# Kernel tuning notes

Measured on AMD Instinct MI355X. Metric: run time of the kernel, lower is better.

The kernel has to match this reference:

```python
import jax, jax.numpy as jnp
import numpy as np
import math

D_MODEL = 1024
EXPAND = 2
D_INNER = D_MODEL * EXPAND  # 2048
D_STATE = 16
DT_RANK = max(1, (D_MODEL + 15) // 16)  # 64
K = 4  # conv kernel size
B, S = 2, 2048


def silu(v):
    return v * jax.nn.sigmoid(v)


def setup_inputs() -> dict:
    key = jax.random.key(0)
    ks = jax.random.split(key, 12)
    sc = lambda fan_in: 1.0 / math.sqrt(fan_in)
    x = jax.random.normal(ks[0], (B, S, D_MODEL), dtype=jnp.float32)
    Win = jax.random.normal(ks[1], (D_MODEL, 2 * D_INNER), dtype=jnp.float32) * sc(D_MODEL)
    Wconv = jax.random.normal(ks[2], (D_INNER, 1, K), dtype=jnp.float32) * sc(K)
    bconv = jax.random.normal(ks[3], (D_INNER,), dtype=jnp.float32) * 0.01
    Wx = jax.random.normal(ks[4], (D_INNER, DT_RANK + 2 * D_STATE), dtype=jnp.float32) * sc(D_INNER)
    Wdt = jax.random.normal(ks[5], (DT_RANK, D_INNER), dtype=jnp.float32) * sc(DT_RANK)
    # dt_proj bias init: inverse-softplus of dt ~ LogUniform[1e-3, 1e-1]
    dt = jnp.exp(jax.random.uniform(ks[6], (D_INNER,)) * (math.log(0.1) - math.log(0.001)) + math.log(0.001))
    dt = jnp.clip(dt, 0.0001, None)
    bdt = dt + jnp.log(-jnp.expm1(-dt))
    a = jnp.arange(1, D_STATE + 1, dtype=jnp.float32)[None, :].repeat(D_INNER, axis=0)
    a = a + jax.random.uniform(ks[7], a.shape) * 0.1
    A_log = jnp.log(a)
    Dp = jnp.ones((D_INNER,), dtype=jnp.float32)
    Wout = jax.random.normal(ks[8], (D_INNER, D_MODEL), dtype=jnp.float32) * sc(D_INNER)
    return {"x": x, "Win": Win, "Wconv": Wconv, "bconv": bconv, "Wx": Wx,
            "Wdt": Wdt, "bdt": bdt, "A_log": A_log, "Dp": Dp, "Wout": Wout}


def causal_dw_conv(x, Wconv, bconv):
    # x: [B, S, C] -> depthwise causal conv along S
    xc = jnp.transpose(x, (0, 2, 1))  # [B, C, S]
    y = jax.lax.conv_general_dilated(
        xc, Wconv, window_strides=(1,), padding=[(K - 1, 0)],
        feature_group_count=D_INNER,
        dimension_numbers=("NCH", "OIH", "NCH"))
    y = y + bconv[None, :, None]
    return jnp.transpose(y, (0, 2, 1))  # [B, S, C]


def selective_scan(u, delta, b_term, c_term, A_log, Dp):
    # u, delta: [B,S,Di]; b_term, c_term: [B,S,Ds]
    a = -jnp.exp(A_log)  # [Di, Ds]
    delta_a = jnp.exp(delta[..., None] * a[None, None])            # [B,S,Di,Ds] fp32
    delta_b_u = (delta * u)[..., None] * b_term[:, :, None, :]     # [B,S,Di,Ds]
    du = u * Dp[None, None, :]                                     # [B,S,Di]
    # time-major for scan
    dA = jnp.transpose(delta_a, (1, 0, 2, 3))
    dBu = jnp.transpose(delta_b_u, (1, 0, 2, 3))
    c_t = jnp.transpose(c_term, (1, 0, 2))
    du_t = jnp.transpose(du, (1, 0, 2))

    def step(state, inp):
        dA_t, dBu_t, c, duv = inp
        state = dA_t * state + dBu_t                  # [B,Di,Ds]
        y = jnp.einsum("bdn,bn->bd", state, c) + duv  # [B,Di]
        return state, y

    init = jnp.zeros((u.shape[0], D_INNER, D_STATE), dtype=jnp.float32)
    _, ys = jax.lax.scan(step, init, (dA, dBu, c_t, du_t))
    return jnp.transpose(ys, (1, 0, 2))  # [B,S,Di]


def reference(x, Win, Wconv, bconv, Wx, Wdt, bdt, A_log, Dp, Wout):
    xz = x @ Win                              # [B,S,2*Di]
    x_branch, z_branch = jnp.split(xz, 2, axis=-1)
    x_branch = silu(causal_dw_conv(x_branch, Wconv, bconv))
    params = x_branch @ Wx                    # [B,S,R+2*Ds]
    delta, b_term, c_term = jnp.split(params, [DT_RANK, DT_RANK + D_STATE], axis=-1)
    delta = jax.nn.softplus(delta @ Wdt + bdt)
    y = selective_scan(x_branch, delta, b_term, c_term, A_log, Dp)
    y = y * silu(z_branch)
    return y @ Wout
```

## Files before the change

### kernel.cpp

```cpp
#include <hip/hip_runtime.h>

typedef unsigned short u16;
typedef _Float16 f16;
typedef f16 f16x8 __attribute__((ext_vector_type(8)));
typedef u16 u16x8 __attribute__((ext_vector_type(8)));
typedef short s16x8 __attribute__((ext_vector_type(8)));
typedef float f32x2 __attribute__((ext_vector_type(2)));
typedef float f32x4 __attribute__((ext_vector_type(4)));
typedef float f32x8 __attribute__((ext_vector_type(8)));

#define T_TOK 4096
#define B_SZ 2
#define S_LEN 2048
#define DMODEL 1024
#define DI 2048
#define DS 16
#define RNK 64
#define NCH 64
#define CLEN 32
#define LDXZ 4096
#define SK 8
#define SK4 4
#define PRM_SLICE (4096 * 128)
#define OUT_SLICE (4096 * 1024)
#define LOG2E 1.4426950408889634f

#define GLOAD_LDS16(gp, lp)                                                                   \
  __builtin_amdgcn_global_load_lds((const __attribute__((address_space(1))) void*)(gp),       \
                                   (__attribute__((address_space(3))) void*)(lp), 16, 0, 0)

__device__ __forceinline__ float b2f(u16 v) { return __uint_as_float(((unsigned)v) << 16); }
__device__ __forceinline__ u16 f2b(float f) {
  unsigned u = __float_as_uint(f);
  return (u16)((u + 0x7fffu + ((u >> 16) & 1u)) >> 16);
}
__device__ __forceinline__ float fexp2(float x) {
#if __has_builtin(__builtin_amdgcn_exp2f)
  return __builtin_amdgcn_exp2f(x);
#else
  return exp2f(x);
#endif
}
__device__ __forceinline__ int dtype_of(const void* dp) {
  unsigned v = *(const unsigned*)dp;
  return (v == 0x3F800000u) ? 0 : (v == 0x3C003C00u) ? 2 : 1;
}
__device__ __forceinline__ float load_any(const void* p, size_t i, int flag) {
  if (flag == 0) return ((const float*)p)[i];
  if (flag == 1) return b2f(((const u16*)p)[i]);
  return (float)((const f16*)p)[i];
}

__device__ __forceinline__ void tr_tile(const void* __restrict__ src, void* __restrict__ dst,
                                        int R, int C, int Cpad, int f, int bx, int by, int ob) {
  __shared__ f16 t[32][33];
  int c0 = bx * 32, r0 = by * 32;
  int tx = threadIdx.x & 31, ty = threadIdx.x >> 5;
#pragma unroll
  for (int i = ty; i < 32; i += 8) {
    int r = r0 + i, c = c0 + tx;
    float v = (r < R && c < C) ? load_any(src, (size_t)r * C + c, f) : 0.f;
    t[i][tx] = (f16)v;
  }
  __syncthreads();
#pragma unroll
  for (int i = ty; i < 32; i += 8) {
    int c = c0 + i, r = r0 + tx;
    if (c < Cpad && r < R) {
      if (ob) ((u16*)dst)[(size_t)c * R + r] = f2b((float)t[tx][i]);
      else ((f16*)dst)[(size_t)c * R + r] = t[tx][i];
    }
  }
}

__global__ __launch_bounds__(256) void k_prep(const void* __restrict__ Wconv, const void* __restrict__ bconv,
                                              const void* __restrict__ bdt, const void* __restrict__ A_log,
                                              const void* __restrict__ Dp, const void* __restrict__ Wx,
                                              const void* __restrict__ Wdt, const void* __restrict__ Win,
                                              const void* __restrict__ x, f16* __restrict__ WxT,
                                              f16* __restrict__ WdtT, u16* __restrict__ WinTb,
                                              u16* __restrict__ xhb, float* __restrict__ a_f,
                                              float* __restrict__ wconv_f, float* __restrict__ bconv_f,
                                              float* __restrict__ bdt_f, float* __restrict__ dp_f,
                                              int* __restrict__ flag) {
  int f = dtype_of(Dp);
  int bid = blockIdx.x, t = threadIdx.x;
  if (bid < 128) {
    int i = bid * 256 + t;
    a_f[i] = -__expf(load_any(A_log, i, f)) * LOG2E;
  } else if (bid < 160) {
    int i = (bid - 128) * 256 + t;
    wconv_f[i] = load_any(Wconv, i, f);
  } else if (bid < 168) {
    int i = (bid - 160) * 256 + t;
    bconv_f[i] = load_any(bconv, i, f);
  } else if (bid < 176) {
    int i = (bid - 168) * 256 + t;
    bdt_f[i] = load_any(bdt, i, f);
  } else if (bid < 184) {
    int i = (bid - 176) * 256 + t;
    dp_f[i] = load_any(Dp, i, f);
  } else if (bid == 184) {
    if (t == 0) *flag = f;
  } else if (bid < 441) {
    int id = bid - 185;
    tr_tile(Wx, WxT, 2048, 96, 128, f, id & 3, id >> 2, 0);
  } else if (bid < 569) {
    int id = bid - 441;
    tr_tile(Wdt, WdtT, 64, 2048, 2048, f, id & 63, id >> 6, 0);
  } else if (bid < 4665) {
    int id = bid - 569;
    tr_tile(Win, WinTb, 1024, 4096, 4096, f, id & 127, id >> 7, 1);
  } else {
    if (f == 1) return;
    size_t i = (size_t)(bid - 4665) * 2048 + (size_t)t * 8;
    u16x8 o;
    if (f == 0) {
      const float* s = (const float*)x + i;
#pragma unroll
      for (int j = 0; j < 8; ++j) o[j] = f2b(s[j]);
    } else {
      const f16* s = (const f16*)x + i;
#pragma unroll
      for (int j = 0; j < 8; ++j) o[j] = f2b((float)s[j]);
    }
    *(u16x8*)(xhb + i) = o;
  }
}

__global__ __launch_bounds__(256) void k_transpose16(const void* __restrict__ src, f16* __restrict__ dst,
                                                     int R, int C, int Cpad, const void* __restrict__ Dp) {
  tr_tile(src, dst, R, C, Cpad, dtype_of(Dp), blockIdx.x, blockIdx.y, 0);
}

__global__ __launch_bounds__(512) void k_gemm1(const void* __restrict__ x0, const u16* __restrict__ xhb,
                                               const u16* __restrict__ Bw, f16* __restrict__ C,
                                               const int* __restrict__ flag) {
  constexpr int LD = 1024, LDC = LDXZ, NT = 16, NP = NT / 2;
  __shared__ __align__(16) u16 lds[8 * 8192];
  const u16* A = (*flag == 1) ? (const u16*)x0 : xhb;
  const int tid = threadIdx.x;
  const int wv = tid >> 6, ln = tid & 63;
  const int quad = ln >> 4, l16 = ln & 15;
  const int wr = wv >> 2, wc = wv & 3;
  const int m0 = blockIdx.y * 256, n0 = blockIdx.x * 256;
  const int rr = tid >> 3;
  const int cc = (tid & 7) ^ (rr & 7);
  const u16* aBase = A + (size_t)m0 * LD + cc * 8;
  const u16* bBase = Bw + (size_t)n0 * LD + cc * 8;
  const int brow = ((tid >> 8) << 6) + (rr & 31);
  u16* const dBase = lds + wv * 512;
  auto stageA = [&](int tile, int mq) {
    const u16* s = aBase + (size_t)(mq * 64 + rr) * LD + tile * 64;
    u16* d = dBase + ((tile & 1) * 4 + mq) * 8192;
    GLOAD_LDS16(s, d);
    GLOAD_LDS16(s + 128 * LD, d + 4096);
  };
  auto stageB = [&](int tile, int nq) {
    const u16* s = bBase + (size_t)(brow + nq * 32) * LD + tile * 64;
    u16* d = dBase + ((tile & 1) * 4 + 2 + nq) * 8192;
    GLOAD_LDS16(s, d);
    GLOAD_LDS16(s + 128 * LD, d + 4096);
  };
  const int rxor = (l16 & 7) << 3;
  f32x4 acc[8][4] = {};
  stageA(0, 0); stageB(0, 1); stageB(0, 0); stageA(0, 1);
  stageA(1, 0); stageB(1, 1);
  asm volatile("s_waitcnt vmcnt(4)" ::: "memory");
  __builtin_amdgcn_s_barrier();
  s16x8 af[4][2], bf[2][2];
  for (int pr = 0; pr < NP; ++pr) {
    const int t0 = 2 * pr;
    const bool more = (pr < NP - 1);
#pragma unroll
    for (int ph = 0; ph < 8; ++ph) {
      const int slot = ph >> 2, q = ph & 3;
      const int mq = q >> 1, nq = (q >> 1) ^ (q & 1);
      const u16* Ar = lds + (slot * 4 + mq) * 8192;
      const u16* Br = lds + (slot * 4 + 2 + nq) * 8192;
      if (q == 0 || q == 2) {
#pragma unroll
        for (int i = 0; i < 4; ++i) {
          const int ra = wr * 64 + i * 16 + l16;
#pragma unroll
          for (int kk = 0; kk < 2; ++kk)
            af[i][kk] = *(const s16x8*)(Ar + ra * 64 + ((kk * 32 + quad * 8) ^ rxor));
        }
      }
      if (q != 2) {
#pragma unroll
        for (int j = 0; j < 2; ++j) {
          const int rb = wc * 32 + j * 16 + l16;
#pragma unroll
          for (int kk = 0; kk < 2; ++kk)
            bf[j][kk] = *(const s16x8*)(Br + rb * 64 + ((kk * 32 + quad * 8) ^ rxor));
        }
      }
      if (ph == 0) stageB(t0 + 1, 0);
      else if (ph == 1) stageA(t0 + 1, 1);
      else if (more) {
        if (ph == 2) stageA(t0 + 2, 0);
        else if (ph == 3) stageB(t0 + 2, 1);
        else if (ph == 4) stageB(t0 + 2, 0);
        else if (ph == 5) stageA(t0 + 2, 1);
        else if (ph == 6) stageA(t0 + 3, 0);
        else stageB(t0 + 3, 1);
      }
      __builtin_amdgcn_s_barrier();
      asm volatile("s_waitcnt lgkmcnt(0)" ::: "memory");
      __builtin_amdgcn_sched_barrier(0);
      __builtin_amdgcn_s_setprio(1);
#pragma unroll
      for (int kk = 0; kk < 2; ++kk)
#pragma unroll
        for (int i = 0; i < 4; ++i)
#pragma unroll
          for (int j = 0; j < 2; ++j)
            acc[mq * 4 + i][nq * 2 + j] = __builtin_amdgcn_mfma_f32_16x16x32_bf16(
                af[i][kk], bf[j][kk], acc[mq * 4 + i][nq * 2 + j], 0, 0, 0);
      __builtin_amdgcn_s_setprio(0);
      if (ph == 3) {
        if (more) asm volatile("s_waitcnt vmcnt(6)" ::: "memory");
        else asm volatile("s_waitcnt vmcnt(2)" ::: "memory");
      } else if (ph == 5) {
        if (more) asm volatile("s_waitcnt vmcnt(8)" ::: "memory");
        else asm volatile("s_waitcnt vmcnt(0)" ::: "memory");
      } else if (ph == 7) {
        if (more) asm volatile("s_waitcnt vmcnt(4)" ::: "memory");
        else asm volatile("s_waitcnt vmcnt(0)" ::: "memory");
      }
      __builtin_amdgcn_s_barrier();
    }
  }
#pragma unroll
  for (int i = 0; i < 8; ++i)
#pragma unroll
    for (int j = 0; j < 4; ++j)
#pragma unroll
      for (int r = 0; r < 4; ++r) {
        const int row = m0 + wr * 128 + i * 16 + quad * 4 + r;
        const int col = n0 + wc * 64 + j * 16 + l16;
        C[(size_t)row * LDC + col] = (f16)acc[i][j][r];
      }
}

template <int BM, int BN, int EPI>
__global__ __launch_bounds__(256) void k_gemm2(const f16* __restrict__ A, const f16* __restrict__ B,
                                               void* __restrict__ Cv, const float* __restrict__ bias,
                                               const int* __restrict__ flag,
                                               int klen, int lda, int ldb, int ldc) {
  constexpr int WM = BM / 2, WN = BN / 2;
  constexpr int FM = WM / 16, FN = WN / 16;
  __shared__ __align__(16) f16 As[2 * BM * 32];
  __shared__ __align__(16) f16 Bs[2 * BN * 32];
  const int tid = threadIdx.x;
  const int wv = tid >> 6, ln = tid & 63;
  const int quad = ln >> 4, l16 = ln & 15;
  const int lrow = ln >> 2;
  const int lch = (((ln & 3) ^ ((ln >> 3) & 3))) * 8;
  const int m0 = blockIdx.y * BM, n0 = blockIdx.x * BN;
  const int wm = (wv & 1) * WM, wn = (wv >> 1) * WN;
  const int kbase = blockIdx.z * klen;
  const int qsw = (quad ^ ((l16 >> 1) & 3)) * 8;
  f32x4 acc[FM][FN] = {};
  for (int kk = 0; kk < klen; kk += 64) {
    const int k0 = kbase + kk;
    __syncthreads();
#pragma unroll
    for (int h = 0; h < 2; ++h) {
#pragma unroll
      for (int i = 0; i < BM / 64; ++i) {
        int r0 = wv * (BM / 4) + i * 16;
        GLOAD_LDS16(A + (size_t)(m0 + r0 + lrow) * lda + k0 + h * 32 + lch, As + h * BM * 32 + r0 * 32);
      }
#pragma unroll
      for (int i = 0; i < BN / 64; ++i) {
        int r0 = wv * (BN / 4) + i * 16;
        GLOAD_LDS16(B + (size_t)(n0 + r0 + lrow) * ldb + k0 + h * 32 + lch, Bs + h * BN * 32 + r0 * 32);
      }
    }
    __syncthreads();
#pragma unroll
    for (int h = 0; h < 2; ++h) {
      f16x8 af[FM], bf[FN];
#pragma unroll
      for (int i = 0; i < FM; ++i) af[i] = *(const f16x8*)(As + h * BM * 32 + (wm + i * 16 + l16) * 32 + qsw);
#pragma unroll
      for (int j = 0; j < FN; ++j) bf[j] = *(const f16x8*)(Bs + h * BN * 32 + (wn + j * 16 + l16) * 32 + qsw);
#pragma unroll
      for (int i = 0; i < FM; ++i)
#pragma unroll
        for (int j = 0; j < FN; ++j)
          acc[i][j] = __builtin_amdgcn_mfma_f32_16x16x32_f16(af[i], bf[j], acc[i][j], 0, 0, 0);
    }
  }
  int dflag = 1;
  if constexpr (EPI == 2) dflag = *flag;
  f16* Cz = (f16*)Cv;
  if constexpr (EPI == 4) Cz = (f16*)Cv + (size_t)blockIdx.z * PRM_SLICE;
  if constexpr (EPI == 5) Cz = (f16*)Cv + (size_t)blockIdx.z * OUT_SLICE;
#pragma unroll
  for (int i = 0; i < FM; ++i)
#pragma unroll
    for (int j = 0; j < FN; ++j)
#pragma unroll
      for (int r = 0; r < 4; ++r) {
        int row = m0 + wm + i * 16 + quad * 4 + r;
        int col = n0 + wn + j * 16 + l16;
        size_t ci = (size_t)row * ldc + col;
        float v = acc[i][j][r];
        if constexpr (EPI == 3) {
          v += bias[row];
          v = (v > 20.f) ? v : log1pf(__expf(v));
          size_t di2 = ((size_t)(row << 1) + (col >> 11)) * (size_t)LDXZ + (col & 2047);
          Cz[di2] = (f16)v;
        } else if constexpr (EPI == 2) {
          if (dflag == 0) ((float*)Cv)[ci] = v;
          else if (dflag == 1) ((u16*)Cv)[ci] = f2b(v);
          else ((f16*)Cv)[ci] = (f16)v;
        } else {
          Cz[ci] = (f16)v;
        }
      }
}

__global__ __launch_bounds__(256) void k_sum_prm(const f16* __restrict__ parts, f16* __restrict__ prm,
                                                 float* __restrict__ prmBC) {
  size_t i = (size_t)(blockIdx.x * 256 + threadIdx.x) * 8;
  int col0 = (int)(i & 127);
  if (col0 >= 96) return;
  float s[8] = {};
#pragma unroll
  for (int z = 0; z < SK; ++z) {
    f16x8 v = *(const f16x8*)(parts + (size_t)z * PRM_SLICE + i);
#pragma unroll
    for (int j = 0; j < 8; ++j) s[j] += (float)v[j];
  }
  if (col0 < 64) {
    f16x8 o;
#pragma unroll
    for (int j = 0; j < 8; ++j) o[j] = (f16)s[j];
    *(f16x8*)(prm + i) = o;
  } else {
    size_t tok = i >> 7;
    f32x8 of;
#pragma unroll
    for (int j = 0; j < 8; ++j) of[j] = s[j];
    *(f32x8*)(prmBC + tok * 32 + (col0 - 64)) = of;
  }
}

__global__ __launch_bounds__(256) void k_sum_out(const f16* __restrict__ parts, void* __restrict__ out,
                                                 const int* __restrict__ flag) {
  size_t i = (size_t)(blockIdx.x * 256 + threadIdx.x) * 8;
  float s[8] = {};
#pragma unroll
  for (int z = 0; z < SK4; ++z) {
    f16x8 v = *(const f16x8*)(parts + (size_t)z * OUT_SLICE + i);
#pragma unroll
    for (int j = 0; j < 8; ++j) s[j] += (float)v[j];
  }
  int f = *flag;
  if (f == 0) {
    f32x8 o;
#pragma unroll
    for (int j = 0; j < 8; ++j) o[j] = s[j];
    *(f32x8*)((float*)out + i) = o;
  } else if (f == 1) {
    u16x8 o;
#pragma unroll
    for (int j = 0; j < 8; ++j) o[j] = f2b(s[j]);
    *(u16x8*)((u16*)out + i) = o;
  } else {
    f16x8 o;
#pragma unroll
    for (int j = 0; j < 8; ++j) o[j] = (f16)s[j];
    *(f16x8*)((f16*)out + i) = o;
  }
}

__global__ __launch_bounds__(256) void k_conv_silu(const f16* __restrict__ xz, const float* __restrict__ Wconv,
                                                   const float* __restrict__ bconv, f16* __restrict__ xc) {
  int t = blockIdx.x;
  int s = t & (S_LEN - 1);
  int d8 = threadIdx.x * 8;
  float w[4][8];
#pragma unroll
  for (int i = 0; i < 8; ++i)
#pragma unroll
    for (int j = 0; j < 4; ++j) w[j][i] = Wconv[(d8 + i) * 4 + j];
  float acc[8];
#pragma unroll
  for (int i = 0; i < 8; ++i) acc[i] = bconv[d8 + i];
#pragma unroll
  for (int j = 0; j < 4; ++j) {
    int sl = s - 3 + j;
    if (sl >= 0) {
      f16x8 xv = *(const f16x8*)(xz + (size_t)(t - 3 + j) * LDXZ + d8);
#pragma unroll
      for (int i = 0; i < 8; ++i) acc[i] = fmaf((float)xv[i], w[j][i], acc[i]);
    }
  }
  f16x8 o;
#pragma unroll
  for (int i = 0; i < 8; ++i) {
    float v = acc[i];
    o[i] = (f16)(v / (1.f + __expf(-v)));
  }
  *(f16x8*)(xc + (size_t)t * DI + d8) = o;
}

__global__ __launch_bounds__(256) void k_scan_passA(const f16* __restrict__ dltT, const f16* __restrict__ u,
                                                    const float* __restrict__ prmBC, const float* __restrict__ a_f,
                                                    f16* __restrict__ lcs, float* __restrict__ sumdv) {
  __shared__ __align__(16) f16 u_lds[CLEN][128];
  __shared__ __align__(16) float b_lds[CLEN][16];
  const int tid = threadIdx.x;
  int g = blockIdx.x * 256 + tid;
  int nh = g & 1, p = g >> 1;
  int d = p & (DI - 1);
  int c = (p >> 11) & (NCH - 1);
  int b = p >> 17;
  const int d0 = d & ~127;
  const int t0 = b * S_LEN + c * CLEN;
  {
    const f16* up0 = u + (size_t)t0 * DI + d0;
#pragma unroll
    for (int rep = 0; rep < 2; ++rep) {
      int chunk = rep * 256 + tid;
      int row = chunk >> 4, c16 = chunk & 15;
      *(f16x8*)&u_lds[row][c16 * 8] = *(const f16x8*)(up0 + (size_t)row * DI + c16 * 8);
    }
    const float* bp0 = prmBC + (size_t)t0 * 32;
    int row = tid >> 3, c2 = tid & 7;
    *(f32x2*)&b_lds[row][c2 * 2] = *(const f32x2*)(bp0 + row * 32 + c2 * 2);
  }
  const f16* dp = dltT + (size_t)(2 * d + b) * LDXZ + c * CLEN;
  f16x8 dlv[4];
#pragma unroll
  for (int q = 0; q < 4; ++q) dlv[q] = *(const f16x8*)(dp + q * 8);
  f32x4 a0 = *(const f32x4*)(a_f + d * DS + nh * 8);
  f32x4 a1 = *(const f32x4*)(a_f + d * DS + nh * 8 + 4);
  float a[8] = {a0[0], a0[1], a0[2], a0[3], a1[0], a1[1], a1[2], a1[3]};
  __syncthreads();
  const int dd = d - d0;
  float st[8] = {};
  float sumd = 0.f;
#pragma unroll
  for (int s = 0; s < CLEN; ++s) {
    float dl = (float)dlv[s >> 3][s & 7];
    float uv = (float)u_lds[s][dd];
    f32x4 bv0 = *(const f32x4*)&b_lds[s][nh * 8];
    f32x4 bv1 = *(const f32x4*)&b_lds[s][nh * 8 + 4];
    sumd += dl;
    float dbu = dl * uv;
#pragma unroll
    for (int j = 0; j < 8; ++j) {
      float e = fexp2(dl * a[j]);
      float bj = (j < 4) ? bv0[j & 3] : bv1[j & 3];
      st[j] = fmaf(e, st[j], dbu * bj);
    }
  }
  f16x8 o;
#pragma unroll
  for (int j = 0; j < 8; ++j) o[j] = (f16)st[j];
  *(f16x8*)(lcs + (size_t)p * DS + nh * 8) = o;
  if (nh == 0) sumdv[p] = sumd;
}

__global__ __launch_bounds__(256) void k_scan_passB(f16* __restrict__ lcs, const float* __restrict__ sumdv,
                                                    const float* __restrict__ a_f) {
  int g = blockIdx.x * 256 + threadIdx.x;
  int n = g & 15, d = (g >> 4) & (DI - 1), b = g >> 15;
  float an = a_f[d * DS + n];
  const size_t base = (size_t)b * NCH * DI + d;
  float lf[4], sf[4];
#pragma unroll
  for (int q = 0; q < 4; ++q) {
    size_t pq = base + (size_t)q * DI;
    lf[q] = (float)lcs[pq * DS + n];
    sf[q] = sumdv[pq];
  }
  float init = 0.f;
#pragma unroll
  for (int c = 0; c < NCH; ++c) {
    size_t pc = base + (size_t)c * DI;
    float l = lf[c & 3], sd = sf[c & 3];
    if (c + 4 < NCH) {
      size_t pn = base + (size_t)(c + 4) * DI;
      lf[c & 3] = (float)lcs[pn * DS + n];
      sf[c & 3] = sumdv[pn];
    }
    lcs[pc * DS + n] = (f16)init;
    init = fexp2(sd * an) * init + l;
  }
}

__global__ __launch_bounds__(256) void k_scan_passC(const f16* __restrict__ dltT, const f16* __restrict__ u,
                                                    const float* __restrict__ prmBC, const float* __restrict__ a_f,
                                                    const float* __restrict__ dp_f, const f16* __restrict__ lcs,
                                                    f16* __restrict__ xz) {
  __shared__ __align__(16) f16 u_lds[CLEN][128];
  __shared__ __align__(16) f16 z_lds[CLEN][128];
  __shared__ __align__(16) float bc_lds[CLEN][32];
  const int tid = threadIdx.x;
  int g = blockIdx.x * 256 + tid;
  int nh = g & 1, p = g >> 1;
  int d = p & (DI - 1);
  int c = (p >> 11) & (NCH - 1);
  int b = p >> 17;
  const int d0 = d & ~127;
  const int t0 = b * S_LEN + c * CLEN;
  f16* const zp0 = xz + (size_t)t0 * LDXZ + DI + d0;
  {
    const f16* up0 = u + (size_t)t0 * DI + d0;
#pragma unroll
    for (int rep = 0; rep < 2; ++rep) {
      int chunk = rep * 256 + tid;
      int row = chunk >> 4, c16 = chunk & 15;
      *(f16x8*)&u_lds[row][c16 * 8] = *(const f16x8*)(up0 + (size_t)row * DI + c16 * 8);
      *(f16x8*)&z_lds[row][c16 * 8] = *(const f16x8*)(zp0 + (size_t)row * LDXZ + c16 * 8);
    }
    ((f32x4*)bc_lds)[tid] = ((const f32x4*)(prmBC + (size_t)t0 * 32))[tid];
  }
  const f16* dp = dltT + (size_t)(2 * d + b) * LDXZ + c * CLEN;
  f16x8 dlv[4];
#pragma unroll
  for (int q = 0; q < 4; ++q) dlv[q] = *(const f16x8*)(dp + q * 8);
  f32x4 a0 = *(const f32x4*)(a_f + d * DS + nh * 8);
  f32x4 a1 = *(const f32x4*)(a_f + d * DS + nh * 8 + 4);
  float a[8] = {a0[0], a0[1], a0[2], a0[3], a1[0], a1[1], a1[2], a1[3]};
  float st[8];
  f16x8 iv = *(const f16x8*)(lcs + (size_t)p * DS + nh * 8);
#pragma unroll
  for (int j = 0; j < 8; ++j) st[j] = (float)iv[j];
  float dpv = dp_f[d];
  __syncthreads();
  const int dd = d - d0;
#pragma unroll
  for (int s = 0; s < CLEN; ++s) {
    float dl = (float)dlv[s >> 3][s & 7];
    float uv = (float)u_lds[s][dd];
    float z = (float)z_lds[s][dd];
    f32x4 bv0 = *(const f32x4*)&bc_lds[s][nh * 8];
    f32x4 bv1 = *(const f32x4*)&bc_lds[s][nh * 8 + 4];
    f32x4 cv0 = *(const f32x4*)&bc_lds[s][16 + nh * 8];
    f32x4 cv1 = *(const f32x4*)&bc_lds[s][16 + nh * 8 + 4];
    float dbu = dl * uv;
    float part = (nh == 0) ? uv * dpv : 0.f;
#pragma unroll
    for (int j = 0; j < 8; ++j) {
      float e = fexp2(dl * a[j]);
      float bj = (j < 4) ? bv0[j & 3] : bv1[j & 3];
      float cj = (j < 4) ? cv0[j & 3] : cv1[j & 3];
      st[j] = fmaf(e, st[j], dbu * bj);
      part = fmaf(st[j], cj, part);
    }
    part += __shfl_xor(part, 1, 64);
    if (nh == 0) {
      float sg = 1.f / (1.f + __expf(-z));
      z_lds[s][dd] = (f16)(part * z * sg);
    }
  }
  __syncthreads();
#pragma unroll
  for (int rep = 0; rep < 2; ++rep) {
    int chunk = rep * 256 + tid;
    int row = chunk >> 4, c16 = chunk & 15;
    *(f16x8*)(zp0 + (size_t)row * LDXZ + c16 * 8) = *(const f16x8*)&z_lds[row][c16 * 8];
  }
}

extern "C" void kernel_launch(void* const* d_in, const int* in_sizes, int n_in,
                              void* d_out, int out_size, void* d_ws, size_t ws_size,
                              hipStream_t stream) {
  const void* x = d_in[0];
  const void* Win = d_in[1];
  const void* Wconv = d_in[2];
  const void* bconv = d_in[3];
  const void* Wx = d_in[4];
  const void* Wdt = d_in[5];
  const void* bdt = d_in[6];
  const void* A_log = d_in[7];
  const void* Dp = d_in[8];
  const void* Wout = d_in[9];
  (void)in_sizes; (void)n_in; (void)out_size; (void)ws_size;

  const size_t KB = 1024, MB = 1024 * 1024;
  char* ws = (char*)d_ws;
  f16* xzh = (f16*)ws;
  u16* xhb = (u16*)(ws + 32 * MB);
  f16* xch = (f16*)(ws + 32 * MB);
  u16* WinTb = (u16*)(ws + 48 * MB);
  f16* parts = (f16*)(ws + 48 * MB);
  f16* lcs = (f16*)(ws + 48 * MB);
  f16* WoutT = (f16*)(ws + 48 * MB);
  float* sumd = (float*)(ws + 56 * MB);
  f16* prm = (f16*)(ws + 57 * MB);
  float* prmBC = (float*)(ws + 58 * MB);
  f16* WxT = (f16*)(ws + 58 * MB + 512 * KB);
  f16* WdtT = (f16*)(ws + 59 * MB);
  float* a_f = (float*)(ws + 59 * MB + 256 * KB);
  float* wconv_f = (float*)(ws + 59 * MB + 384 * KB);
  float* bconv_f = (float*)(ws + 59 * MB + 416 * KB);
  float* bdt_f = (float*)(ws + 59 * MB + 424 * KB);
  float* dp_f = (float*)(ws + 59 * MB + 432 * KB);
  int* flag = (int*)(ws + 59 * MB + 440 * KB);
  f16* parts4 = (f16*)(ws + 64 * MB);

  k_prep<<<6713, 256, 0, stream>>>(Wconv, bconv, bdt, A_log, Dp, Wx, Wdt, Win, x,
                                   WxT, WdtT, WinTb, xhb, a_f, wconv_f, bconv_f, bdt_f, dp_f, flag);

  k_gemm1<<<dim3(16, 16), 512, 0, stream>>>(x, xhb, WinTb, xzh, flag);
  k_conv_silu<<<T_TOK, 256, 0, stream>>>(xzh, wconv_f, bconv_f, xch);
  k_gemm2<64, 128, 4><<<dim3(1, 4096 / 64, SK), 256, 0, stream>>>(
      xch, WxT, parts, nullptr, flag, 2048 / SK, 2048, 2048, 128);
  k_sum_prm<<<PRM_SLICE / 8 / 256, 256, 0, stream>>>(parts, prm, prmBC);
  k_gemm2<128, 128, 3><<<dim3(4096 / 128, 2048 / 128), 256, 0, stream>>>(
      WdtT, prm, xzh, bdt_f, flag, 64, 64, 128, 0);
  k_scan_passA<<<(B_SZ * NCH * DI * 2) / 256, 256, 0, stream>>>(xzh, xch, prmBC, a_f, lcs, sumd);
  k_scan_passB<<<(B_SZ * DI * DS) / 256, 256, 0, stream>>>(lcs, sumd, a_f);
  k_scan_passC<<<(B_SZ * NCH * DI * 2) / 256, 256, 0, stream>>>(xzh, xch, prmBC, a_f, dp_f, lcs, xzh);
  k_transpose16<<<dim3(1024 / 32, 2048 / 32), 256, 0, stream>>>(Wout, WoutT, 2048, 1024, 1024, Dp);
  k_gemm2<64, 128, 5><<<dim3(1024 / 128, 4096 / 64, SK4), 256, 0, stream>>>(
      xzh + DI, WoutT, parts4, nullptr, flag, 2048 / SK4, LDXZ, 2048, 1024);
  k_sum_out<<<OUT_SLICE / 8 / 256, 256, 0, stream>>>(parts4, d_out, flag);
}
```

Measured before the change: 330.8 us.

## Scan passes: one thread per channel with all 16 states, B/C via scalar loads

Scan passes A and C change from two threads per channel (8 states each, joined by a shuffle) to one thread per channel holding all 16 states, with each block covering 256 channels. B/C coefficients are read straight from global memory at block-uniform addresses, which can become scalar loads, instead of being staged in LDS. This removes the cross-lane shuffle, the nh-predicated work and the LDS traffic for B/C. In exchange the grid is half as large and each thread carries more registers, so there is less parallelism and possibly lower occupancy.

```diff
diff --git a/kernel.cpp b/kernel.cpp
--- a/kernel.cpp
+++ b/kernel.cpp
@@ -413,59 +413,57 @@
 __global__ __launch_bounds__(256) void k_scan_passA(const f16* __restrict__ dltT, const f16* __restrict__ u,
                                                     const float* __restrict__ prmBC, const float* __restrict__ a_f,
                                                     f16* __restrict__ lcs, float* __restrict__ sumdv) {
-  __shared__ __align__(16) f16 u_lds[CLEN][128];
-  __shared__ __align__(16) float b_lds[CLEN][16];
+  __shared__ __align__(16) f16 u_lds[CLEN][256];
   const int tid = threadIdx.x;
-  int g = blockIdx.x * 256 + tid;
-  int nh = g & 1, p = g >> 1;
-  int d = p & (DI - 1);
-  int c = (p >> 11) & (NCH - 1);
-  int b = p >> 17;
-  const int d0 = d & ~127;
+  const int blk = blockIdx.x;
+  const int dblk = blk & 7;
+  const int c = (blk >> 3) & (NCH - 1);
+  const int b = blk >> 9;
+  const int d = dblk * 256 + tid;
   const int t0 = b * S_LEN + c * CLEN;
   {
-    const f16* up0 = u + (size_t)t0 * DI + d0;
-#pragma unroll
-    for (int rep = 0; rep < 2; ++rep) {
+    const f16* up0 = u + (size_t)t0 * DI + dblk * 256;
+#pragma unroll
+    for (int rep = 0; rep < 4; ++rep) {
       int chunk = rep * 256 + tid;
-      int row = chunk >> 4, c16 = chunk & 15;
-      *(f16x8*)&u_lds[row][c16 * 8] = *(const f16x8*)(up0 + (size_t)row * DI + c16 * 8);
-    }
-    const float* bp0 = prmBC + (size_t)t0 * 32;
-    int row = tid >> 3, c2 = tid & 7;
-    *(f32x2*)&b_lds[row][c2 * 2] = *(const f32x2*)(bp0 + row * 32 + c2 * 2);
-  }
+      int row = chunk >> 5, c32 = chunk & 31;
+      *(f16x8*)&u_lds[row][c32 * 8] = *(const f16x8*)(up0 + (size_t)row * DI + c32 * 8);
+    }
+  }
+  const float* __restrict__ bcp = prmBC + (size_t)t0 * 32;
   const f16* dp = dltT + (size_t)(2 * d + b) * LDXZ + c * CLEN;
   f16x8 dlv[4];
 #pragma unroll
   for (int q = 0; q < 4; ++q) dlv[q] = *(const f16x8*)(dp + q * 8);
-  f32x4 a0 = *(const f32x4*)(a_f + d * DS + nh * 8);
-  f32x4 a1 = *(const f32x4*)(a_f + d * DS + nh * 8 + 4);
-  float a[8] = {a0[0], a0[1], a0[2], a0[3], a1[0], a1[1], a1[2], a1[3]};
+  float a[16];
+#pragma unroll
+  for (int q = 0; q < 4; ++q) {
+    f32x4 av = *(const f32x4*)(a_f + d * DS + q * 4);
+#pragma unroll
+    for (int j = 0; j < 4; ++j) a[q * 4 + j] = av[j];
+  }
   __syncthreads();
-  const int dd = d - d0;
-  float st[8] = {};
+  float st[16] = {};
   float sumd = 0.f;
 #pragma unroll
   for (int s = 0; s < CLEN; ++s) {
     float dl = (float)dlv[s >> 3][s & 7];
-    float uv = (float)u_lds[s][dd];
-    f32x4 bv0 = *(const f32x4*)&b_lds[s][nh * 8];
-    f32x4 bv1 = *(const f32x4*)&b_lds[s][nh * 8 + 4];
+    float uv = (float)u_lds[s][tid];
     sumd += dl;
     float dbu = dl * uv;
 #pragma unroll
-    for (int j = 0; j < 8; ++j) {
+    for (int j = 0; j < 16; ++j) {
       float e = fexp2(dl * a[j]);
-      float bj = (j < 4) ? bv0[j & 3] : bv1[j & 3];
-      st[j] = fmaf(e, st[j], dbu * bj);
-    }
-  }
-  f16x8 o;
-#pragma unroll
-  for (int j = 0; j < 8; ++j) o[j] = (f16)st[j];
-  *(f16x8*)(lcs + (size_t)p * DS + nh * 8) = o;
-  if (nh == 0) sumdv[p] = sumd;
+      st[j] = fmaf(e, st[j], dbu * bcp[s * 32 + j]);
+    }
+  }
+  size_t p = (size_t)b * NCH * DI + (size_t)c * DI + d;
+  f16x8 o0, o1;
+#pragma unroll
+  for (int j = 0; j < 8; ++j) { o0[j] = (f16)st[j]; o1[j] = (f16)st[j + 8]; }
+  *(f16x8*)(lcs + p * DS) = o0;
+  *(f16x8*)(lcs + p * DS + 8) = o1;
+  sumdv[p] = sumd;
 }
 
 __global__ __launch_bounds__(256) void k_scan_passB(f16* __restrict__ lcs, const float* __restrict__ sumdv,
@@ -500,74 +498,70 @@
                                                     const float* __restrict__ prmBC, const float* __restrict__ a_f,
                                                     const float* __restrict__ dp_f, const f16* __restrict__ lcs,
                                                     f16* __restrict__ xz) {
-  __shared__ __align__(16) f16 u_lds[CLEN][128];
-  __shared__ __align__(16) f16 z_lds[CLEN][128];
-  __shared__ __align__(16) float bc_lds[CLEN][32];
+  __shared__ __align__(16) f16 u_lds[CLEN][256];
+  __shared__ __align__(16) f16 z_lds[CLEN][256];
   const int tid = threadIdx.x;
-  int g = blockIdx.x * 256 + tid;
-  int nh = g & 1, p = g >> 1;
-  int d = p & (DI - 1);
-  int c = (p >> 11) & (NCH - 1);
-  int b = p >> 17;
-  const int d0 = d & ~127;
+  const int blk = blockIdx.x;
+  const int dblk = blk & 7;
+  const int c = (blk >> 3) & (NCH - 1);
+  const int b = blk >> 9;
+  const int d = dblk * 256 + tid;
   const int t0 = b * S_LEN + c * CLEN;
-  f16* const zp0 = xz + (size_t)t0 * LDXZ + DI + d0;
+  f16* const zp0 = xz + (size_t)t0 * LDXZ + DI + dblk * 256;
   {
-    const f16* up0 = u + (size_t)t0 * DI + d0;
-#pragma unroll
-    for (int rep = 0; rep < 2; ++rep) {
+    const f16* up0 = u + (size_t)t0 * DI + dblk * 256;
+#pragma unroll
+    for (int rep = 0; rep < 4; ++rep) {
       int chunk = rep * 256 + tid;
-      int row = chunk >> 4, c16 = chunk & 15;
-      *(f16x8*)&u_lds[row][c16 * 8] = *(const f16x8*)(up0 + (size_t)row * DI + c16 * 8);
-      *(f16x8*)&z_lds[row][c16 * 8] = *(const f16x8*)(zp0 + (size_t)row * LDXZ + c16 * 8);
-    }
-    ((f32x4*)bc_lds)[tid] = ((const f32x4*)(prmBC + (size_t)t0 * 32))[tid];
-  }
+      int row = chunk >> 5, c32 = chunk & 31;
+      *(f16x8*)&u_lds[row][c32 * 8] = *(const f16x8*)(up0 + (size_t)row * DI + c32 * 8);
+      *(f16x8*)&z_lds[row][c32 * 8] = *(const f16x8*)(zp0 + (size_t)row * LDXZ + c32 * 8);
+    }
+  }
+  const float* __restrict__ bcp = prmBC + (size_t)t0 * 32;
   const f16* dp = dltT + (size_t)(2 * d + b) * LDXZ + c * CLEN;
   f16x8 dlv[4];
 #pragma unroll
   for (int q = 0; q < 4; ++q) dlv[q] = *(const f16x8*)(dp + q * 8);
-  f32x4 a0 = *(const f32x4*)(a_f + d * DS + nh * 8);
-  f32x4 a1 = *(const f32x4*)(a_f + d * DS + nh * 8 + 4);
-  float a[8] = {a0[0], a0[1], a0[2], a0[3], a1[0], a1[1], a1[2], a1[3]};
-  float st[8];
-  f16x8 iv = *(const f16x8*)(lcs + (size_t)p * DS + nh * 8);
-#pragma unroll
-  for (int j = 0; j < 8; ++j) st[j] = (float)iv[j];
-  float dpv = dp_f[d];
+  float a[16];
+#pragma unroll
+  for (int q = 0; q < 4; ++q) {
+    f32x4 av = *(const f32x4*)(a_f + d * DS + q * 4);
+#pragma unroll
+    for (int j = 0; j < 4; ++j) a[q * 4 + j] = av[j];
+  }
+  size_t p = (size_t)b * NCH * DI + (size_t)c * DI + d;
+  float st[16];
+  {
+    f16x8 iv0 = *(const f16x8*)(lcs + p * DS);
+    f16x8 iv1 = *(const f16x8*)(lcs + p * DS + 8);
+#pragma unroll
+    for (int j = 0; j < 8; ++j) { st[j] = (float)iv0[j]; st[j + 8] = (float)iv1[j]; }
+  }
+  const float dpv = dp_f[d];
   __syncthreads();
-  const int dd = d - d0;
 #pragma unroll
   for (int s = 0; s < CLEN; ++s) {
     float dl = (float)dlv[s >> 3][s & 7];
-    float uv = (float)u_lds[s][dd];
-    float z = (float)z_lds[s][dd];
-    f32x4 bv0 = *(const f32x4*)&bc_lds[s][nh * 8];
-    f32x4 bv1 = *(const f32x4*)&bc_lds[s][nh * 8 + 4];
-    f32x4 cv0 = *(const f32x4*)&bc_lds[s][16 + nh * 8];
-    f32x4 cv1 = *(const f32x4*)&bc_lds[s][16 + nh * 8 + 4];
+    float uv = (float)u_lds[s][tid];
+    float z = (float)z_lds[s][tid];
     float dbu = dl * uv;
-    float part = (nh == 0) ? uv * dpv : 0.f;
-#pragma unroll
-    for (int j = 0; j < 8; ++j) {
+    float part = uv * dpv;
+#pragma unroll
+    for (int j = 0; j < 16; ++j) {
       float e = fexp2(dl * a[j]);
-      float bj = (j < 4) ? bv0[j & 3] : bv1[j & 3];
-      float cj = (j < 4) ? cv0[j & 3] : cv1[j & 3];
-      st[j] = fmaf(e, st[j], dbu * bj);
-      part = fmaf(st[j], cj, part);
-    }
-    part += __shfl_xor(part, 1, 64);
-    if (nh == 0) {
-      float sg = 1.f / (1.f + __expf(-z));
-      z_lds[s][dd] = (f16)(part * z * sg);
-    }
+      st[j] = fmaf(e, st[j], dbu * bcp[s * 32 + j]);
+      part = fmaf(st[j], bcp[s * 32 + 16 + j], part);
+    }
+    float sg = 1.f / (1.f + __expf(-z));
+    z_lds[s][tid] = (f16)(part * z * sg);
   }
   __syncthreads();
 #pragma unroll
-  for (int rep = 0; rep < 2; ++rep) {
+  for (int rep = 0; rep < 4; ++rep) {
     int chunk = rep * 256 + tid;
-    int row = chunk >> 4, c16 = chunk & 15;
-    *(f16x8*)(zp0 + (size_t)row * LDXZ + c16 * 8) = *(const f16x8*)&z_lds[row][c16 * 8];
+    int row = chunk >> 5, c32 = chunk & 31;
+    *(f16x8*)(zp0 + (size_t)row * LDXZ + c32 * 8) = *(const f16x8*)&z_lds[row][c32 * 8];
   }
 }
 
@@ -618,9 +612,9 @@
   k_sum_prm<<<PRM_SLICE / 8 / 256, 256, 0, stream>>>(parts, prm, prmBC);
   k_gemm2<128, 128, 3><<<dim3(4096 / 128, 2048 / 128), 256, 0, stream>>>(
       WdtT, prm, xzh, bdt_f, flag, 64, 64, 128, 0);
-  k_scan_passA<<<(B_SZ * NCH * DI * 2) / 256, 256, 0, stream>>>(xzh, xch, prmBC, a_f, lcs, sumd);
+  k_scan_passA<<<B_SZ * NCH * (DI / 256), 256, 0, stream>>>(xzh, xch, prmBC, a_f, lcs, sumd);
   k_scan_passB<<<(B_SZ * DI * DS) / 256, 256, 0, stream>>>(lcs, sumd, a_f);
-  k_scan_passC<<<(B_SZ * NCH * DI * 2) / 256, 256, 0, stream>>>(xzh, xch, prmBC, a_f, dp_f, lcs, xzh);
+  k_scan_passC<<<B_SZ * NCH * (DI / 256), 256, 0, stream>>>(xzh, xch, prmBC, a_f, dp_f, lcs, xzh);
   k_transpose16<<<dim3(1024 / 32, 2048 / 32), 256, 0, stream>>>(Wout, WoutT, 2048, 1024, 1024, Dp);
   k_gemm2<64, 128, 5><<<dim3(1024 / 128, 4096 / 64, SK4), 256, 0, stream>>>(
       xzh + DI, WoutT, parts4, nullptr, flag, 2048 / SK4, LDXZ, 2048, 1024);
```

Result: slower. 343.9 us (+4.0%).

## Use 256x256 pipelined split-K GEMM kernel for output projection

Applied to the files above, without the earlier changes.

Replaces the 64x128 split-K output projection GEMM with a new 256x256-tile, 512-thread kernel. It stages tiles into LDS through direct global-to-LDS loads with double buffering, uses an 8-phase interleaved load/compute schedule, and raises wave priority around the MFMA blocks. The larger tiles are meant to improve data reuse and overlap memory traffic with compute. The trade-off is fewer blocks (256 rather than 2048) and heavy LDS use, which may hurt occupancy.

```diff
diff --git a/kernel.cpp b/kernel.cpp
--- a/kernel.cpp
+++ b/kernel.cpp
@@ -244,6 +244,118 @@
       }
 }
 
+__global__ __launch_bounds__(512) void k_gemm8p(const f16* __restrict__ A, const f16* __restrict__ B,
+                                                f16* __restrict__ Cp, int lda, int ldb, int ldc,
+                                                int ksl, int nt) {
+  __shared__ __align__(16) u16 lds[8 * 8192];
+  const int np = nt >> 1;
+  const int tid = threadIdx.x;
+  const int wv = tid >> 6, ln = tid & 63;
+  const int quad = ln >> 4, l16 = ln & 15;
+  const int wr = wv >> 2, wc = wv & 3;
+  const int m0 = blockIdx.y * 256, n0 = blockIdx.x * 256;
+  const int kbase = blockIdx.z * ksl;
+  const int rr = tid >> 3;
+  const int cc = (tid & 7) ^ (rr & 7);
+  const u16* aBase = (const u16*)A + (size_t)m0 * lda + kbase + cc * 8;
+  const u16* bBase = (const u16*)B + (size_t)n0 * ldb + kbase + cc * 8;
+  const int brow = ((tid >> 8) << 6) + (rr & 31);
+  u16* const dBase = lds + wv * 512;
+  auto stageA = [&](int tile, int mq) {
+    const u16* s = aBase + (size_t)(mq * 64 + rr) * lda + tile * 64;
+    u16* d = dBase + ((tile & 1) * 4 + mq) * 8192;
+    GLOAD_LDS16(s, d);
+    GLOAD_LDS16(s + (size_t)128 * lda, d + 4096);
+  };
+  auto stageB = [&](int tile, int nq) {
+    const u16* s = bBase + (size_t)(brow + nq * 32) * ldb + tile * 64;
+    u16* d = dBase + ((tile & 1) * 4 + 2 + nq) * 8192;
+    GLOAD_LDS16(s, d);
+    GLOAD_LDS16(s + (size_t)128 * ldb, d + 4096);
+  };
+  const int rxor = (l16 & 7) << 3;
+  f32x4 acc[8][4] = {};
+  stageA(0, 0); stageB(0, 1); stageB(0, 0); stageA(0, 1);
+  stageA(1, 0); stageB(1, 1);
+  asm volatile("s_waitcnt vmcnt(4)" ::: "memory");
+  __builtin_amdgcn_s_barrier();
+  f16x8 af[4][2], bf[2][2];
+  for (int pr = 0; pr < np; ++pr) {
+    const int t0 = 2 * pr;
+    const bool more = (pr < np - 1);
+#pragma unroll
+    for (int ph = 0; ph < 8; ++ph) {
+      const int slot = ph >> 2, q = ph & 3;
+      const int mq = q >> 1, nq = (q >> 1) ^ (q & 1);
+      const u16* Ar = lds + (slot * 4 + mq) * 8192;
+      const u16* Br = lds + (slot * 4 + 2 + nq) * 8192;
+      if (q == 0 || q == 2) {
+#pragma unroll
+        for (int i = 0; i < 4; ++i) {
+          const int ra = wr * 64 + i * 16 + l16;
+#pragma unroll
+          for (int kk = 0; kk < 2; ++kk)
+            af[i][kk] = *(const f16x8*)(Ar + ra * 64 + ((kk * 32 + quad * 8) ^ rxor));
+        }
+      }
+      if (q != 2) {
+#pragma unroll
+        for (int j = 0; j < 2; ++j) {
+          const int rb = wc * 32 + j * 16 + l16;
+#pragma unroll
+          for (int kk = 0; kk < 2; ++kk)
+            bf[j][kk] = *(const f16x8*)(Br + rb * 64 + ((kk * 32 + quad * 8) ^ rxor));
+        }
+      }
+      if (ph == 0) stageB(t0 + 1, 0);
+      else if (ph == 1) stageA(t0 + 1, 1);
+      else if (more) {
+        if (ph == 2) stageA(t0 + 2, 0);
+        else if (ph == 3) stageB(t0 + 2, 1);
+        else if (ph == 4) stageB(t0 + 2, 0);
+        else if (ph == 5) stageA(t0 + 2, 1);
+        else if (ph == 6) stageA(t0 + 3, 0);
+        else stageB(t0 + 3, 1);
+      }
+      __builtin_amdgcn_s_barrier();
+      asm volatile("s_waitcnt lgkmcnt(0)" ::: "memory");
+      __builtin_amdgcn_sched_barrier(0);
+      __builtin_amdgcn_s_setprio(1);
+#pragma unroll
+      for (int kk = 0; kk < 2; ++kk)
+#pragma unroll
+        for (int i = 0; i < 4; ++i)
+#pragma unroll
+          for (int j = 0; j < 2; ++j)
+            acc[mq * 4 + i][nq * 2 + j] = __builtin_amdgcn_mfma_f32_16x16x32_f16(
+                af[i][kk], bf[j][kk], acc[mq * 4 + i][nq * 2 + j], 0, 0, 0);
+      __builtin_amdgcn_s_setprio(0);
+      if (ph == 3) {
+        if (more) asm volatile("s_waitcnt vmcnt(6)" ::: "memory");
+        else asm volatile("s_waitcnt vmcnt(2)" ::: "memory");
+      } else if (ph == 5) {
+        if (more) asm volatile("s_waitcnt vmcnt(8)" ::: "memory");
+        else asm volatile("s_waitcnt vmcnt(0)" ::: "memory");
+      } else if (ph == 7) {
+        if (more) asm volatile("s_waitcnt vmcnt(4)" ::: "memory");
+        else asm volatile("s_waitcnt vmcnt(0)" ::: "memory");
+      }
+      __builtin_amdgcn_s_barrier();
+    }
+  }
+  f16* Cz = Cp + (size_t)blockIdx.z * OUT_SLICE;
+#pragma unroll
+  for (int i = 0; i < 8; ++i)
+#pragma unroll
+    for (int j = 0; j < 4; ++j)
+#pragma unroll
+      for (int r = 0; r < 4; ++r) {
+        const int row = m0 + wr * 128 + i * 16 + quad * 4 + r;
+        const int col = n0 + wc * 64 + j * 16 + l16;
+        Cz[(size_t)row * ldc + col] = (f16)acc[i][j][r];
+      }
+}
+
 template <int BM, int BN, int EPI>
 __global__ __launch_bounds__(256) void k_gemm2(const f16* __restrict__ A, const f16* __restrict__ B,
                                                void* __restrict__ Cv, const float* __restrict__ bias,
@@ -298,7 +410,6 @@
   if constexpr (EPI == 2) dflag = *flag;
   f16* Cz = (f16*)Cv;
   if constexpr (EPI == 4) Cz = (f16*)Cv + (size_t)blockIdx.z * PRM_SLICE;
-  if constexpr (EPI == 5) Cz = (f16*)Cv + (size_t)blockIdx.z * OUT_SLICE;
 #pragma unroll
   for (int i = 0; i < FM; ++i)
 #pragma unroll
@@ -622,7 +733,7 @@
   k_scan_passB<<<(B_SZ * DI * DS) / 256, 256, 0, stream>>>(lcs, sumd, a_f);
   k_scan_passC<<<(B_SZ * NCH * DI * 2) / 256, 256, 0, stream>>>(xzh, xch, prmBC, a_f, dp_f, lcs, xzh);
   k_transpose16<<<dim3(1024 / 32, 2048 / 32), 256, 0, stream>>>(Wout, WoutT, 2048, 1024, 1024, Dp);
-  k_gemm2<64, 128, 5><<<dim3(1024 / 128, 4096 / 64, SK4), 256, 0, stream>>>(
-      xzh + DI, WoutT, parts4, nullptr, flag, 2048 / SK4, LDXZ, 2048, 1024);
+  k_gemm8p<<<dim3(1024 / 256, 4096 / 256, SK4), 512, 0, stream>>>(
+      xzh + DI, WoutT, parts4, LDXZ, 2048, 1024, 2048 / SK4, 2048 / SK4 / 64);
   k_sum_out<<<OUT_SLICE / 8 / 256, 256, 0, stream>>>(parts4, d_out, flag);
 }
```

New measurement: 323.3 us. -2.3%, faster.
